# Performance work log

Hardware: AMD Instinct MI355X
Metric: run time of the kernel (lower is better)

## Reference

```python
import jax, jax.numpy as jnp
import numpy as np

EPS = 1e-8  # torch cosine_similarity eps


def setup_inputs() -> dict:
    key = jax.random.key(0)
    k1, k2, k3 = jax.random.split(key, 3)
    N, D, n_classes = 512, 512, 10
    prediction = jax.random.normal(k1, (N, D), dtype=jnp.float32)
    # raw (pre-softplus) learnable distances, n_classes - 1 of them
    distances_raw = jax.random.uniform(k2, (n_classes - 1,), dtype=jnp.float32)
    target = jax.random.randint(k3, (N,), 0, n_classes)
    return {"prediction": prediction, "distances_raw": distances_raw, "target": target}


def reference(prediction, distances_raw, target):
    N = prediction.shape[0]
    # cosine similarity matrix [N, N]
    norms = jnp.linalg.norm(prediction, axis=1, keepdims=True)
    xn = prediction / jnp.maximum(norms, EPS)
    cos = xn @ xn.T

    same = target[:, None] == target[None, :]
    eye = jnp.eye(N, dtype=bool)
    positives = same & ~eye          # same-class pairs, excluding self
    negatives = ~same                # different-class pairs (diag excluded since same)

    # ordinal class positions on a line; pairwise class-center distances
    pos_d = jax.nn.softplus(distances_raw)
    class_pos = jnp.concatenate([jnp.zeros((1,), cos.dtype), jnp.cumsum(pos_d)])
    dist_matrix = jnp.abs(class_pos[:, None] - class_pos[None, :])
    margins = dist_matrix[target[:, None], target[None, :]]
    margins = jnp.where(negatives, margins, 0.0)

    # term[i, j, k] = relu(cos[i,j] + margin[i,j] - cos[i,k]),
    # valid only when (i,j) is a negative pair and (i,k) is a positive pair.
    term = jax.nn.relu((cos + margins)[:, :, None] - cos[:, None, :])  # [i,j,k]
    term = term * negatives[:, :, None].astype(cos.dtype) * positives[:, None, :].astype(cos.dtype)

    S = term.sum(axis=1)                                  # [i, k]
    n_neg = negatives.sum(axis=1).astype(cos.dtype)       # [i]
    count = positives.astype(cos.dtype) * n_neg[:, None]  # [i, k] valid-pair counts
    loss_ik = S / jnp.maximum(count, 1.0)

    # aggregate over positive anchors k, then mean over samples i
    tot = (loss_ik * (count > 0)).sum(axis=1) / jnp.maximum(count.sum(axis=1), 1.0)
    return tot.mean()
```

## Files before the change

### kernel.cpp

```cpp
#include <hip/hip_runtime.h>
#include <math.h>

#define N 512
#define D 512
#define NC 10
#define EPSF 1e-8f

__global__ __launch_bounds__(256) void k_gram(
    const float* __restrict__ pred,
    const float* __restrict__ dist_raw,
    float* __restrict__ G,
    float* __restrict__ inv_n,
    float* __restrict__ class_pos,
    float* __restrict__ out) {
  __shared__ float As[32][36];
  __shared__ float Bs[32][36];

  const int bi = blockIdx.y, bj = blockIdx.x;
  const int t = threadIdx.x;
  const int lr = t >> 3;
  const int lk = (t & 7) << 2;
  const int ty = t >> 4;
  const int tx = t & 15;

  const float* Ag = pred + (size_t)(bi * 32 + lr) * D + lk;
  const float* Bg = pred + (size_t)(bj * 32 + lr) * D + lk;

  float c00 = 0.f, c01 = 0.f, c10 = 0.f, c11 = 0.f;

  float4 av = *(const float4*)(Ag);
  float4 bv = *(const float4*)(Bg);

  for (int kb = 0; kb < D; kb += 32) {
    *(float4*)(&As[lr][lk]) = av;
    *(float4*)(&Bs[lr][lk]) = bv;
    __syncthreads();
    if (kb + 32 < D) {
      av = *(const float4*)(Ag + kb + 32);
      bv = *(const float4*)(Bg + kb + 32);
    }
#pragma unroll
    for (int k = 0; k < 32; k += 4) {
      float4 a0 = *(const float4*)(&As[ty][k]);
      float4 a1 = *(const float4*)(&As[ty + 16][k]);
      float4 b0 = *(const float4*)(&Bs[tx][k]);
      float4 b1 = *(const float4*)(&Bs[tx + 16][k]);
      c00 += a0.x * b0.x + a0.y * b0.y + a0.z * b0.z + a0.w * b0.w;
      c01 += a0.x * b1.x + a0.y * b1.y + a0.z * b1.z + a0.w * b1.w;
      c10 += a1.x * b0.x + a1.y * b0.y + a1.z * b0.z + a1.w * b0.w;
      c11 += a1.x * b1.x + a1.y * b1.y + a1.z * b1.z + a1.w * b1.w;
    }
    __syncthreads();
  }

  const int row0 = bi * 32 + ty, row1 = row0 + 16;
  const int col0 = bj * 32 + tx, col1 = col0 + 16;
  G[(size_t)row0 * N + col0] = c00;
  G[(size_t)row0 * N + col1] = c01;
  G[(size_t)row1 * N + col0] = c10;
  G[(size_t)row1 * N + col1] = c11;

  if (bi == bj && tx == ty) {
    inv_n[row0] = 1.0f / fmaxf(sqrtf(c00), EPSF);
    inv_n[row1] = 1.0f / fmaxf(sqrtf(c11), EPSF);
  }
  if (bi == 0 && bj == 0 && t == 0) {
    out[0] = 0.0f;
    float acc = 0.0f;
    class_pos[0] = 0.0f;
    for (int c = 0; c < NC - 1; c++) {
      acc += log1pf(expf(dist_raw[c]));
      class_pos[c + 1] = acc;
    }
  }
}

__global__ __launch_bounds__(256) void k_rows(
    const float* __restrict__ G,
    const int* __restrict__ target,
    const float* __restrict__ inv_n,
    const float* __restrict__ class_pos,
    float* __restrict__ out) {
  const int i = blockIdx.x;
  const int tid = threadIdx.x;

  __shared__ float s_a[N];
  __shared__ float s_p[N];
  __shared__ float s_cp[NC];
  __shared__ int s_np, s_nn;

  if (tid == 0) { s_np = 0; s_nn = 0; }
  if (tid < NC) s_cp[tid] = class_pos[tid];
  __syncthreads();

  const int ti = target[i];
  const float inv_i = inv_n[i];
  const float cpi = s_cp[ti];

  for (int j = tid; j < N; j += 256) {
    float cosv = G[(size_t)i * N + j] * inv_i * inv_n[j];
    int tj = target[j];
    if (tj != ti) {
      float m = fabsf(cpi - s_cp[tj]);
      int idx = atomicAdd(&s_nn, 1);
      s_a[idx] = cosv + m;
    } else if (j != i) {
      int idx = atomicAdd(&s_np, 1);
      s_p[idx] = cosv;
    }
  }
  __syncthreads();

  const int np = s_np, nn = s_nn;
  float a0 = (tid < nn) ? s_a[tid] : -1e30f;
  float a1 = (tid + 256 < nn) ? s_a[tid + 256] : -1e30f;
  float acc = 0.0f;
  for (int kk = 0; kk < np; kk++) {
    float ck = s_p[kk];
    acc += fmaxf(a0 - ck, 0.0f) + fmaxf(a1 - ck, 0.0f);
  }

  for (int off = 32; off > 0; off >>= 1) acc += __shfl_down(acc, off);
  __shared__ float s_part[4];
  if ((tid & 63) == 0) s_part[tid >> 6] = acc;
  __syncthreads();
  if (tid == 0) {
    float total = s_part[0] + s_part[1] + s_part[2] + s_part[3];
    if (np > 0 && nn > 0) {
      float r = total / ((float)nn * (float)nn * (float)np);
      atomicAdd(out, r / (float)N);
    }
  }
}

extern "C" void kernel_launch(void* const* d_in, const int* in_sizes, int n_in,
                              void* d_out, int out_size, void* d_ws, size_t ws_size,
                              hipStream_t stream) {
  const float* pred = (const float*)d_in[0];
  const float* dist_raw = (const float*)d_in[1];
  const int* target = (const int*)d_in[2];
  float* out = (float*)d_out;

  float* G = (float*)d_ws;
  float* inv_n = G + (size_t)N * N;
  float* class_pos = inv_n + N;

  dim3 ggrid(16, 16);
  k_gram<<<ggrid, 256, 0, stream>>>(pred, dist_raw, G, inv_n, class_pos, out);
  k_rows<<<N, 256, 0, stream>>>(G, target, inv_n, class_pos, out);
}
```

Baseline: 81.67 us.

## Split-K gram with 128x128 register-tiled blocks and partial-slice reduction in row kernel

The gram kernel now uses 128x128 output tiles with an 8x8 per-thread register block and splits the K dimension into 16 slices across blockIdx.z. Each slice writes its own partial N×N matrix, and the row kernel sums the 16 slices on read. Squared norms are accumulated with atomics, and the class-position softplus is moved into every row block, with memsets zeroing the accumulators. This trades much more global traffic (16 partial matrices written and reread) and two extra memset launches for higher arithmetic intensity and better parallelism in the gram stage.

```diff
diff --git a/kernel.cpp b/kernel.cpp
--- a/kernel.cpp
+++ b/kernel.cpp
@@ -4,82 +4,78 @@
 #define N 512
 #define D 512
 #define NC 10
+#define NSLICE 16
+#define KS 32
+#define MP 132
 #define EPSF 1e-8f
 
 __global__ __launch_bounds__(256) void k_gram(
     const float* __restrict__ pred,
-    const float* __restrict__ dist_raw,
-    float* __restrict__ G,
-    float* __restrict__ inv_n,
-    float* __restrict__ class_pos,
-    float* __restrict__ out) {
-  __shared__ float As[32][36];
-  __shared__ float Bs[32][36];
+    float* __restrict__ Gp,
+    float* __restrict__ norm2) {
+  __shared__ __align__(16) float As[KS][MP];
+  __shared__ __align__(16) float Bs[KS][MP];
 
-  const int bi = blockIdx.y, bj = blockIdx.x;
+  const int bj = blockIdx.x, bi = blockIdx.y, s = blockIdx.z;
   const int t = threadIdx.x;
-  const int lr = t >> 3;
-  const int lk = (t & 7) << 2;
-  const int ty = t >> 4;
-  const int tx = t & 15;
+  const int tx = t & 15, ty = t >> 4;
 
-  const float* Ag = pred + (size_t)(bi * 32 + lr) * D + lk;
-  const float* Bg = pred + (size_t)(bj * 32 + lr) * D + lk;
+#pragma unroll
+  for (int j = 0; j < 4; j++) {
+    int f = t + 256 * j;
+    int r = f >> 3;
+    int q = f & 7;
+    float4 va = *(const float4*)(pred + (size_t)(bi * 128 + r) * D + s * KS + q * 4);
+    float4 vb = *(const float4*)(pred + (size_t)(bj * 128 + r) * D + s * KS + q * 4);
+    As[q * 4 + 0][r] = va.x; As[q * 4 + 1][r] = va.y;
+    As[q * 4 + 2][r] = va.z; As[q * 4 + 3][r] = va.w;
+    Bs[q * 4 + 0][r] = vb.x; Bs[q * 4 + 1][r] = vb.y;
+    Bs[q * 4 + 2][r] = vb.z; Bs[q * 4 + 3][r] = vb.w;
+  }
+  __syncthreads();
 
-  float c00 = 0.f, c01 = 0.f, c10 = 0.f, c11 = 0.f;
+  float acc[8][8];
+#pragma unroll
+  for (int r = 0; r < 8; r++)
+#pragma unroll
+    for (int c = 0; c < 8; c++) acc[r][c] = 0.0f;
 
-  float4 av = *(const float4*)(Ag);
-  float4 bv = *(const float4*)(Bg);
-
-  for (int kb = 0; kb < D; kb += 32) {
-    *(float4*)(&As[lr][lk]) = av;
-    *(float4*)(&Bs[lr][lk]) = bv;
-    __syncthreads();
-    if (kb + 32 < D) {
-      av = *(const float4*)(Ag + kb + 32);
-      bv = *(const float4*)(Bg + kb + 32);
-    }
+#pragma unroll 4
+  for (int k = 0; k < KS; k++) {
+    float4 a0 = *(const float4*)(&As[k][ty * 8]);
+    float4 a1 = *(const float4*)(&As[k][ty * 8 + 4]);
+    float4 b0 = *(const float4*)(&Bs[k][tx * 8]);
+    float4 b1 = *(const float4*)(&Bs[k][tx * 8 + 4]);
+    float a[8] = {a0.x, a0.y, a0.z, a0.w, a1.x, a1.y, a1.z, a1.w};
+    float b[8] = {b0.x, b0.y, b0.z, b0.w, b1.x, b1.y, b1.z, b1.w};
 #pragma unroll
-    for (int k = 0; k < 32; k += 4) {
-      float4 a0 = *(const float4*)(&As[ty][k]);
-      float4 a1 = *(const float4*)(&As[ty + 16][k]);
-      float4 b0 = *(const float4*)(&Bs[tx][k]);
-      float4 b1 = *(const float4*)(&Bs[tx + 16][k]);
-      c00 += a0.x * b0.x + a0.y * b0.y + a0.z * b0.z + a0.w * b0.w;
-      c01 += a0.x * b1.x + a0.y * b1.y + a0.z * b1.z + a0.w * b1.w;
-      c10 += a1.x * b0.x + a1.y * b0.y + a1.z * b0.z + a1.w * b0.w;
-      c11 += a1.x * b1.x + a1.y * b1.y + a1.z * b1.z + a1.w * b1.w;
-    }
-    __syncthreads();
+    for (int r = 0; r < 8; r++)
+#pragma unroll
+      for (int c = 0; c < 8; c++) acc[r][c] += a[r] * b[c];
   }
 
-  const int row0 = bi * 32 + ty, row1 = row0 + 16;
-  const int col0 = bj * 32 + tx, col1 = col0 + 16;
-  G[(size_t)row0 * N + col0] = c00;
-  G[(size_t)row0 * N + col1] = c01;
-  G[(size_t)row1 * N + col0] = c10;
-  G[(size_t)row1 * N + col1] = c11;
-
+  float* Gs = Gp + (size_t)s * N * N;
+  const int n0 = bj * 128 + tx * 8;
+#pragma unroll
+  for (int r = 0; r < 8; r++) {
+    int m = bi * 128 + ty * 8 + r;
+    float4 lo = {acc[r][0], acc[r][1], acc[r][2], acc[r][3]};
+    float4 hi = {acc[r][4], acc[r][5], acc[r][6], acc[r][7]};
+    *(float4*)(&Gs[(size_t)m * N + n0]) = lo;
+    *(float4*)(&Gs[(size_t)m * N + n0 + 4]) = hi;
+  }
   if (bi == bj && tx == ty) {
-    inv_n[row0] = 1.0f / fmaxf(sqrtf(c00), EPSF);
-    inv_n[row1] = 1.0f / fmaxf(sqrtf(c11), EPSF);
-  }
-  if (bi == 0 && bj == 0 && t == 0) {
-    out[0] = 0.0f;
-    float acc = 0.0f;
-    class_pos[0] = 0.0f;
-    for (int c = 0; c < NC - 1; c++) {
-      acc += log1pf(expf(dist_raw[c]));
-      class_pos[c + 1] = acc;
-    }
+#pragma unroll
+    for (int r = 0; r < 8; r++)
+      atomicAdd(&norm2[bi * 128 + ty * 8 + r], acc[r][r]);
   }
 }
 
 __global__ __launch_bounds__(256) void k_rows(
-    const float* __restrict__ G,
+    const float* __restrict__ Gp,
     const int* __restrict__ target,
-    const float* __restrict__ inv_n,
-    const float* __restrict__ class_pos,
+    const float* __restrict__ norm2,
+    const float* __restrict__ dist_raw,
     float* __restrict__ out) {
   const int i = blockIdx.x;
   const int tid = threadIdx.x;
@@ -89,16 +85,27 @@
   __shared__ float s_cp[NC];
   __shared__ int s_np, s_nn;
 
-  if (tid == 0) { s_np = 0; s_nn = 0; }
-  if (tid < NC) s_cp[tid] = class_pos[tid];
+  if (tid == 0) {
+    s_np = 0; s_nn = 0;
+    float acc = 0.0f;
+    s_cp[0] = 0.0f;
+    for (int c = 0; c < NC - 1; c++) {
+      acc += log1pf(expf(dist_raw[c]));
+      s_cp[c + 1] = acc;
+    }
+  }
   __syncthreads();
 
   const int ti = target[i];
-  const float inv_i = inv_n[i];
+  const float inv_i = 1.0f / fmaxf(sqrtf(norm2[i]), EPSF);
   const float cpi = s_cp[ti];
 
   for (int j = tid; j < N; j += 256) {
-    float cosv = G[(size_t)i * N + j] * inv_i * inv_n[j];
+    float g = 0.0f;
+#pragma unroll
+    for (int s = 0; s < NSLICE; s++)
+      g += Gp[(size_t)s * N * N + (size_t)i * N + j];
+    float cosv = g * inv_i * (1.0f / fmaxf(sqrtf(norm2[j]), EPSF));
     int tj = target[j];
     if (tj != ti) {
       float m = fabsf(cpi - s_cp[tj]);
@@ -141,11 +148,13 @@
   const int* target = (const int*)d_in[2];
   float* out = (float*)d_out;
 
-  float* G = (float*)d_ws;
-  float* inv_n = G + (size_t)N * N;
-  float* class_pos = inv_n + N;
+  float* Gp = (float*)d_ws;
+  float* norm2 = Gp + (size_t)NSLICE * N * N;
 
-  dim3 ggrid(16, 16);
-  k_gram<<<ggrid, 256, 0, stream>>>(pred, dist_raw, G, inv_n, class_pos, out);
-  k_rows<<<N, 256, 0, stream>>>(G, target, inv_n, class_pos, out);
+  hipMemsetAsync(norm2, 0, N * sizeof(float), stream);
+  hipMemsetAsync(out, 0, sizeof(float), stream);
+
+  dim3 ggrid(4, 4, NSLICE);
+  k_gram<<<ggrid, 256, 0, stream>>>(pred, Gp, norm2);
+  k_rows<<<N, 256, 0, stream>>>(Gp, target, norm2, dist_raw, out);
 }
```

Result: slower. 88.68 us (+8.6%).

## Split Gram K dimension across waves with 4x4 register tiles and LDS reduction

Applied to the files above, without the earlier changes.

The Gram kernel now loads 128-wide K chunks into shared memory and has each of the four waves compute a 32-wide K slice with a 4x4 register tile per thread. The partial sums are then reduced across waves through shared memory and written as float4 stores. This cuts the number of barrier-separated iterations from 16 to 4 and raises arithmetic intensity per LDS load. The class-position softplus/cumsum moves into each k_rows block, which removes the serial single-thread work from the Gram kernel but repeats it in every row block. The trade-off is more shared memory per block (about 52KB), which may lower occupancy.

```diff
diff --git a/kernel.cpp b/kernel.cpp
--- a/kernel.cpp
+++ b/kernel.cpp
@@ -5,81 +5,116 @@
 #define D 512
 #define NC 10
 #define EPSF 1e-8f
+#define PITCH 132
 
 __global__ __launch_bounds__(256) void k_gram(
     const float* __restrict__ pred,
-    const float* __restrict__ dist_raw,
     float* __restrict__ G,
     float* __restrict__ inv_n,
-    float* __restrict__ class_pos,
     float* __restrict__ out) {
-  __shared__ float As[32][36];
-  __shared__ float Bs[32][36];
+  __shared__ __align__(16) float As[32][PITCH];
+  __shared__ __align__(16) float Bs[32][PITCH];
+  __shared__ __align__(16) float red[4][32][36];
 
-  const int bi = blockIdx.y, bj = blockIdx.x;
+  const int bj = blockIdx.x, bi = blockIdx.y;
   const int t = threadIdx.x;
-  const int lr = t >> 3;
-  const int lk = (t & 7) << 2;
-  const int ty = t >> 4;
-  const int tx = t & 15;
+  const int w = t >> 6;
+  const int lane = t & 63;
+  const int tx = lane & 7;
+  const int ty = lane >> 3;
 
-  const float* Ag = pred + (size_t)(bi * 32 + lr) * D + lk;
-  const float* Bg = pred + (size_t)(bj * 32 + lr) * D + lk;
+  const float* Arow = pred + (size_t)(bi * 32) * D;
+  const float* Brow = pred + (size_t)(bj * 32) * D;
 
-  float c00 = 0.f, c01 = 0.f, c10 = 0.f, c11 = 0.f;
+  float acc[4][4];
+#pragma unroll
+  for (int r = 0; r < 4; r++)
+#pragma unroll
+    for (int c = 0; c < 4; c++) acc[r][c] = 0.0f;
 
-  float4 av = *(const float4*)(Ag);
-  float4 bv = *(const float4*)(Bg);
+  const int srow = t >> 5 >= 0 ? 0 : 0;
 
-  for (int kb = 0; kb < D; kb += 32) {
-    *(float4*)(&As[lr][lk]) = av;
-    *(float4*)(&Bs[lr][lk]) = bv;
+  float4 pa[4], pb[4];
+#pragma unroll
+  for (int j = 0; j < 4; j++) {
+    int f = t + 256 * j;
+    int row = f >> 5, k4 = f & 31;
+    pa[j] = *(const float4*)(Arow + (size_t)row * D + k4 * 4);
+    pb[j] = *(const float4*)(Brow + (size_t)row * D + k4 * 4);
+  }
+
+  for (int ch = 0; ch < 4; ch++) {
+#pragma unroll
+    for (int j = 0; j < 4; j++) {
+      int f = t + 256 * j;
+      int row = f >> 5, k4 = f & 31;
+      *(float4*)(&As[row][k4 * 4]) = pa[j];
+      *(float4*)(&Bs[row][k4 * 4]) = pb[j];
+    }
     __syncthreads();
-    if (kb + 32 < D) {
-      av = *(const float4*)(Ag + kb + 32);
-      bv = *(const float4*)(Bg + kb + 32);
+
+    if (ch < 3) {
+      int k0 = (ch + 1) * 128;
+#pragma unroll
+      for (int j = 0; j < 4; j++) {
+        int f = t + 256 * j;
+        int row = f >> 5, k4 = f & 31;
+        pa[j] = *(const float4*)(Arow + (size_t)row * D + k0 + k4 * 4);
+        pb[j] = *(const float4*)(Brow + (size_t)row * D + k0 + k4 * 4);
+      }
     }
+
+    const int kb = w * 32;
 #pragma unroll
-    for (int k = 0; k < 32; k += 4) {
-      float4 a0 = *(const float4*)(&As[ty][k]);
-      float4 a1 = *(const float4*)(&As[ty + 16][k]);
-      float4 b0 = *(const float4*)(&Bs[tx][k]);
-      float4 b1 = *(const float4*)(&Bs[tx + 16][k]);
-      c00 += a0.x * b0.x + a0.y * b0.y + a0.z * b0.z + a0.w * b0.w;
-      c01 += a0.x * b1.x + a0.y * b1.y + a0.z * b1.z + a0.w * b1.w;
-      c10 += a1.x * b0.x + a1.y * b0.y + a1.z * b0.z + a1.w * b0.w;
-      c11 += a1.x * b1.x + a1.y * b1.y + a1.z * b1.z + a1.w * b1.w;
+    for (int kk = 0; kk < 32; kk += 4) {
+      float4 av[4], bv[4];
+#pragma unroll
+      for (int r = 0; r < 4; r++) av[r] = *(const float4*)(&As[ty + 8 * r][kb + kk]);
+#pragma unroll
+      for (int c = 0; c < 4; c++) bv[c] = *(const float4*)(&Bs[tx + 8 * c][kb + kk]);
+#pragma unroll
+      for (int r = 0; r < 4; r++)
+#pragma unroll
+        for (int c = 0; c < 4; c++)
+          acc[r][c] += av[r].x * bv[c].x + av[r].y * bv[c].y +
+                       av[r].z * bv[c].z + av[r].w * bv[c].w;
     }
     __syncthreads();
   }
 
-  const int row0 = bi * 32 + ty, row1 = row0 + 16;
-  const int col0 = bj * 32 + tx, col1 = col0 + 16;
-  G[(size_t)row0 * N + col0] = c00;
-  G[(size_t)row0 * N + col1] = c01;
-  G[(size_t)row1 * N + col0] = c10;
-  G[(size_t)row1 * N + col1] = c11;
+#pragma unroll
+  for (int r = 0; r < 4; r++)
+#pragma unroll
+    for (int c = 0; c < 4; c++)
+      red[w][ty + 8 * r][tx + 8 * c] = acc[r][c];
+  __syncthreads();
 
-  if (bi == bj && tx == ty) {
-    inv_n[row0] = 1.0f / fmaxf(sqrtf(c00), EPSF);
-    inv_n[row1] = 1.0f / fmaxf(sqrtf(c11), EPSF);
+  const int m = t >> 3;
+  const int n4 = (t & 7) * 4;
+  float4 s0 = *(const float4*)(&red[0][m][n4]);
+  float4 s1 = *(const float4*)(&red[1][m][n4]);
+  float4 s2 = *(const float4*)(&red[2][m][n4]);
+  float4 s3 = *(const float4*)(&red[3][m][n4]);
+  float4 s;
+  s.x = (s0.x + s1.x) + (s2.x + s3.x);
+  s.y = (s0.y + s1.y) + (s2.y + s3.y);
+  s.z = (s0.z + s1.z) + (s2.z + s3.z);
+  s.w = (s0.w + s1.w) + (s2.w + s3.w);
+
+  *(float4*)(&G[(size_t)(bi * 32 + m) * N + bj * 32 + n4]) = s;
+
+  if (bi == bj && m >= n4 && m < n4 + 4) {
+    float dv = (&s.x)[m - n4];
+    inv_n[bi * 32 + m] = 1.0f / fmaxf(sqrtf(dv), EPSF);
   }
-  if (bi == 0 && bj == 0 && t == 0) {
-    out[0] = 0.0f;
-    float acc = 0.0f;
-    class_pos[0] = 0.0f;
-    for (int c = 0; c < NC - 1; c++) {
-      acc += log1pf(expf(dist_raw[c]));
-      class_pos[c + 1] = acc;
-    }
-  }
+  if (bi == 0 && bj == 0 && t == 0) out[0] = 0.0f;
 }
 
 __global__ __launch_bounds__(256) void k_rows(
     const float* __restrict__ G,
     const int* __restrict__ target,
     const float* __restrict__ inv_n,
-    const float* __restrict__ class_pos,
+    const float* __restrict__ dist_raw,
     float* __restrict__ out) {
   const int i = blockIdx.x;
   const int tid = threadIdx.x;
@@ -89,8 +124,15 @@
   __shared__ float s_cp[NC];
   __shared__ int s_np, s_nn;
 
-  if (tid == 0) { s_np = 0; s_nn = 0; }
-  if (tid < NC) s_cp[tid] = class_pos[tid];
+  if (tid == 0) {
+    s_np = 0; s_nn = 0;
+    float acc = 0.0f;
+    s_cp[0] = 0.0f;
+    for (int c = 0; c < NC - 1; c++) {
+      acc += log1pf(expf(dist_raw[c]));
+      s_cp[c + 1] = acc;
+    }
+  }
   __syncthreads();
 
   const int ti = target[i];
@@ -101,9 +143,9 @@
     float cosv = G[(size_t)i * N + j] * inv_i * inv_n[j];
     int tj = target[j];
     if (tj != ti) {
-      float m = fabsf(cpi - s_cp[tj]);
+      float mg = fabsf(cpi - s_cp[tj]);
       int idx = atomicAdd(&s_nn, 1);
-      s_a[idx] = cosv + m;
+      s_a[idx] = cosv + mg;
     } else if (j != i) {
       int idx = atomicAdd(&s_np, 1);
       s_p[idx] = cosv;
@@ -143,9 +185,8 @@
 
   float* G = (float*)d_ws;
   float* inv_n = G + (size_t)N * N;
-  float* class_pos = inv_n + N;
 
   dim3 ggrid(16, 16);
-  k_gram<<<ggrid, 256, 0, stream>>>(pred, dist_raw, G, inv_n, class_pos, out);
-  k_rows<<<N, 256, 0, stream>>>(G, target, inv_n, class_pos, out);
+  k_gram<<<ggrid, 256, 0, stream>>>(pred, G, inv_n, out);
+  k_rows<<<N, 256, 0, stream>>>(G, target, inv_n, dist_raw, out);
 }
```

New measurement: 85.53 us. 4.7% more time.
